# Kernel tuning notes

Measured on AMD Instinct MI355X. Metric: run time of the kernel, lower is better.

Reference implementation:

```python
import jax, jax.numpy as jnp
import numpy as np

NH = 16  # matches init kwarg nh


def setup_inputs() -> dict:
    key = jax.random.key(0)
    k1, k2 = jax.random.split(key)
    b, S, T = 4, 4096, 4096
    x = jax.random.normal(k1, (b, S, 1), dtype=jnp.float32)
    coords_rel = jax.random.normal(k2, (2, b, S, T), dtype=jnp.float32)
    return {"x": x, "coords_rel": coords_rel}


def reference(x, coords_rel):
    # coords_rel: [2, b, S, T]; x: [b, S, 1]
    d = jnp.sqrt(coords_rel[0] ** 2 + coords_rel[1] ** 2)            # [b, S, T]
    # torch.topk(d, NH, dim=1, largest=False): smallest NH along source dim, ascending
    neg_vals, idx = jax.lax.top_k(jnp.transpose(-d, (0, 2, 1)), NH)  # [b, T, NH]
    dist_abs = jnp.transpose(-neg_vals, (0, 2, 1))                   # [b, NH, T]
    indices = jnp.transpose(idx, (0, 2, 1))                          # [b, NH, T]
    b, nh, t = dist_abs.shape
    w = 1.0 / (dist_abs + 1e-15) ** 2                                # [b, nh, t]
    denom = w.sum(axis=2)                                            # [b, nh] (sum over t, as in source)
    # faithful reproduction of torch .view(t,b,nh) raw reinterpretation + broadcast divide + .view(b,t,nh)
    w = (w.reshape(t, b, nh) / denom).reshape(b, t, nh)              # [b, t, nh]
    S = x.shape[1]
    idx_btn = indices.reshape(b, t, nh)                              # raw reshape, matches torch .view
    # gather: out[i,j,k] = x[i, idx[i,j,k], 0]  (x.repeat over last dim makes all columns equal)
    xg = jnp.take_along_axis(jnp.broadcast_to(x, (b, S, nh)), idx_btn, axis=1)  # [b, t, nh]
    out = (xg * w).sum(axis=2)                                       # [b, t]
    return out[..., None]                                            # [b, t, 1]
```

## Files before the change

kernel.cpp:

```cpp
#include <hip/hip_runtime.h>

#define B_ 4
#define S_ 4096
#define T_ 4096
#define NH_ 16
#define CPB 32
#define CPW 2
#define ROWS 64
#define NTILE (S_ / ROWS)
#define LDSP 33
#define NCG (T_ / CPB)

typedef unsigned long long u64;

__device__ __forceinline__ float dpp_shr1_f(float v) {
    return __int_as_float(__builtin_amdgcn_update_dpp(
        0, __float_as_int(v), 0x111 , 0xF, 0xF, true));
}
__device__ __forceinline__ int dpp_shr1_i(int v) {
    return __builtin_amdgcn_update_dpp(0, v, 0x111, 0xF, 0xF, true);
}

__global__ __launch_bounds__(1024, 8) void topk_scan(
    const float* __restrict__ coords,
    float* __restrict__ outW,
    int*   __restrict__ outI,
    float* __restrict__ partials)
{
    __shared__ float lds[2][2][ROWS * LDSP];
    __shared__ float red[16 * NH_];

    const int bid  = blockIdx.x;
    const int b    = bid >> 7;
    const int c0   = (bid & (NCG - 1)) * CPB;
    const int tid  = threadIdx.x;
    const int w    = tid >> 6;
    const int lane = tid & 63;

    const size_t plane = (size_t)B_ * S_ * T_;
    const int stid = tid & 511;
    const int srow = stid >> 3;
    const int scol = (stid & 7) * 4;
    const int pl   = (tid >= 512) ? 1 : 0;
    const float* gp = coords + (size_t)b * S_ * T_ + (size_t)srow * T_ + (c0 + scol)
                    + (pl ? plane : (size_t)0);
    float* w0 = &lds[0][pl][srow * LDSP + scol];
    float* w1 = &lds[1][pl][srow * LDSP + scol];

    float lv[CPW]; int li[CPW]; float tau[CPW];
#pragma unroll
    for (int cc = 0; cc < CPW; ++cc) {
        lv[cc]  = __int_as_float(0x7f800000);
        li[cc]  = 0;
        tau[cc] = __int_as_float(0x7f800000);
    }

    float4 r4 = *(const float4*)gp;
    w0[0] = r4.x; w0[1] = r4.y; w0[2] = r4.z; w0[3] = r4.w;
    r4 = *(const float4*)(gp + (size_t)ROWS * T_);
    __syncthreads();

#pragma unroll 1
    for (int k = 0; k < NTILE; ++k) {
        if (k + 1 < NTILE) {
            float* wb = (k & 1) ? w0 : w1;
            wb[0] = r4.x; wb[1] = r4.y; wb[2] = r4.z; wb[3] = r4.w;
        }
        if (k + 2 < NTILE)
            r4 = *(const float4*)(gp + (size_t)(k + 2) * ROWS * T_);

        const float* rb0 = lds[k & 1][0];
        const float* rb1 = lds[k & 1][1];
#pragma unroll
        for (int cc = 0; cc < CPW; ++cc) {
            const int col = w * CPW + cc;
            const float dx = rb0[lane * LDSP + col];
            const float dy = rb1[lane * LDSP + col];
            const float d2 = __fadd_rn(__fmul_rn(dx, dx), __fmul_rn(dy, dy));
            u64 m = __ballot(d2 < tau[cc]);
            while (m) {
                const int src = __ffsll(m) - 1;
                m &= m - 1;
                const float cd = __shfl(d2, src);
                const int   ci = k * ROWS + src;
                const unsigned pm = (unsigned)__ballot(lv[cc] <= cd) & 0xFFFFu;
                const int p = __popc(pm);
                const float uv = dpp_shr1_f(lv[cc]);
                const int   ui = dpp_shr1_i(li[cc]);
                const bool here  = (lane == p);
                const bool shift = (lane > p) && (lane < NH_);
                lv[cc] = here ? cd : (shift ? uv : lv[cc]);
                li[cc] = here ? ci : (shift ? ui : li[cc]);
                tau[cc] = __builtin_amdgcn_readlane(__float_as_int(lv[cc]), NH_ - 1)
                              == 0 ? 0.0f : __int_as_float(
                          __builtin_amdgcn_readlane(__float_as_int(lv[cc]), NH_ - 1));
                m &= __ballot(d2 < tau[cc]);
            }
        }
        __syncthreads();
    }

    float dsum = 0.f;
#pragma unroll
    for (int cc = 0; cc < CPW; ++cc) {
        const int t = c0 + w * CPW + cc;
        if (lane < NH_) {
            const float d = sqrtf(lv[cc]) + 1e-15f;
            const float wv = 1.0f / (d * d);
            outW[((size_t)b * T_ + t) * NH_ + lane] = wv;
            outI[((size_t)b * T_ + t) * NH_ + lane] = li[cc];
            dsum += wv;
        }
    }
    if (lane < NH_) red[w * NH_ + lane] = dsum;
    __syncthreads();
    if (tid < NH_) {
        float s = 0.f;
#pragma unroll
        for (int q = 0; q < 16; ++q) s += red[q * NH_ + tid];
        partials[(size_t)bid * NH_ + tid] = s;
    }
}

__global__ __launch_bounds__(128) void denom_reduce(
    const float* __restrict__ partials, float* __restrict__ denom)
{
    const int q = blockIdx.x;
    const int b = q >> 4, j = q & 15;
    const int g = threadIdx.x;
    __shared__ float sm[128];
    sm[g] = partials[(size_t)(b * NCG + g) * NH_ + j];
    __syncthreads();
    for (int s = 64; s > 0; s >>= 1) {
        if (g < s) sm[g] += sm[g + s];
        __syncthreads();
    }
    if (g == 0) denom[q] = sm[0];
}

__global__ __launch_bounds__(256) void out_kernel(
    const float* __restrict__ x,
    const float* __restrict__ outW,
    const int*   __restrict__ outI,
    const float* __restrict__ denom,
    float* __restrict__ out)
{
    const int gid = blockIdx.x * 256 + threadIdx.x;
    const int i = gid >> 12;
    const int j = gid & 4095;
    const int ih = j >> 8;
    const size_t base = ((size_t)i * T_ + (size_t)(j & 255) * NH_) * NH_ + ih;
    const int dq = (j & 3) * NH_;
    float acc = 0.f;
#pragma unroll
    for (int k = 0; k < NH_; ++k) {
        float w  = outW[base + (size_t)k * NH_];
        int   id = outI[base + (size_t)k * NH_];
        acc += x[i * S_ + id] * w / denom[dq + k];
    }
    out[gid] = acc;
}

extern "C" void kernel_launch(void* const* d_in, const int* in_sizes, int n_in,
                              void* d_out, int out_size, void* d_ws, size_t ws_size,
                              hipStream_t stream) {
    const float* x      = (const float*)d_in[0];
    const float* coords = (const float*)d_in[1];
    float* out = (float*)d_out;

    float* outW     = (float*)d_ws;
    int*   outI     = (int*)(outW + (size_t)B_ * T_ * NH_);
    float* partials = (float*)(outI + (size_t)B_ * T_ * NH_);
    float* denom    = partials + (size_t)(B_ * NCG) * NH_;

    topk_scan   <<<B_ * NCG,      1024, 0, stream>>>(coords, outW, outI, partials);
    denom_reduce<<<64,            128,  0, stream>>>(partials, denom);
    out_kernel  <<<B_ * T_ / 256, 256,  0, stream>>>(x, outW, outI, denom, out);
}
```

Baseline: 144.8 us.

## Compute squared distances at staging time and parallelize output reduction across lanes

The staging threads (now only the first 512) load both coordinate planes, compute dx*dx+dy*dy and write a single distance tile to LDS. This halves the LDS footprint and the per-wave LDS reads in the scan. The candidate broadcast now uses readlane instead of shfl, and the redundant tau zero check is removed. The output kernel uses 16 threads per output with a shuffle reduction, replacing the serial 16-element loop, which launches more threads but exposes more memory parallelism for the gathers.

```diff
diff --git a/kernel.cpp b/kernel.cpp
--- a/kernel.cpp
+++ b/kernel.cpp
@@ -27,7 +27,7 @@
     int*   __restrict__ outI,
     float* __restrict__ partials)
 {
-    __shared__ float lds[2][2][ROWS * LDSP];
+    __shared__ float lds[2][ROWS * LDSP];
     __shared__ float red[16 * NH_];
 
     const int bid  = blockIdx.x;
@@ -38,14 +38,13 @@
     const int lane = tid & 63;
 
     const size_t plane = (size_t)B_ * S_ * T_;
-    const int stid = tid & 511;
-    const int srow = stid >> 3;
-    const int scol = (stid & 7) * 4;
-    const int pl   = (tid >= 512) ? 1 : 0;
-    const float* gp = coords + (size_t)b * S_ * T_ + (size_t)srow * T_ + (c0 + scol)
-                    + (pl ? plane : (size_t)0);
-    float* w0 = &lds[0][pl][srow * LDSP + scol];
-    float* w1 = &lds[1][pl][srow * LDSP + scol];
+    const bool stager = (tid < 512);
+    const int  srow = tid >> 3;
+    const int  scol = (tid & 7) * 4;
+    const float* g0 = coords + (size_t)b * S_ * T_ + (size_t)srow * T_ + (c0 + scol);
+    const float* g1 = g0 + plane;
+    float* wb0 = &lds[0][srow * LDSP + scol];
+    float* wb1 = &lds[1][srow * LDSP + scol];
 
     float lv[CPW]; int li[CPW]; float tau[CPW];
 #pragma unroll
@@ -55,33 +54,45 @@
         tau[cc] = __int_as_float(0x7f800000);
     }
 
-    float4 r4 = *(const float4*)gp;
-    w0[0] = r4.x; w0[1] = r4.y; w0[2] = r4.z; w0[3] = r4.w;
-    r4 = *(const float4*)(gp + (size_t)ROWS * T_);
+    float4 ax, ay;
+    if (stager) {
+        ax = *(const float4*)g0;  ay = *(const float4*)g1;
+        wb0[0] = __fadd_rn(__fmul_rn(ax.x, ax.x), __fmul_rn(ay.x, ay.x));
+        wb0[1] = __fadd_rn(__fmul_rn(ax.y, ax.y), __fmul_rn(ay.y, ay.y));
+        wb0[2] = __fadd_rn(__fmul_rn(ax.z, ax.z), __fmul_rn(ay.z, ay.z));
+        wb0[3] = __fadd_rn(__fmul_rn(ax.w, ax.w), __fmul_rn(ay.w, ay.w));
+        ax = *(const float4*)(g0 + (size_t)ROWS * T_);
+        ay = *(const float4*)(g1 + (size_t)ROWS * T_);
+    }
     __syncthreads();
 
 #pragma unroll 1
     for (int k = 0; k < NTILE; ++k) {
-        if (k + 1 < NTILE) {
-            float* wb = (k & 1) ? w0 : w1;
-            wb[0] = r4.x; wb[1] = r4.y; wb[2] = r4.z; wb[3] = r4.w;
+        if (stager) {
+            if (k + 1 < NTILE) {
+                float* wb = (k & 1) ? wb0 : wb1;
+                wb[0] = __fadd_rn(__fmul_rn(ax.x, ax.x), __fmul_rn(ay.x, ay.x));
+                wb[1] = __fadd_rn(__fmul_rn(ax.y, ax.y), __fmul_rn(ay.y, ay.y));
+                wb[2] = __fadd_rn(__fmul_rn(ax.z, ax.z), __fmul_rn(ay.z, ay.z));
+                wb[3] = __fadd_rn(__fmul_rn(ax.w, ax.w), __fmul_rn(ay.w, ay.w));
+            }
+            if (k + 2 < NTILE) {
+                ax = *(const float4*)(g0 + (size_t)(k + 2) * ROWS * T_);
+                ay = *(const float4*)(g1 + (size_t)(k + 2) * ROWS * T_);
+            }
         }
-        if (k + 2 < NTILE)
-            r4 = *(const float4*)(gp + (size_t)(k + 2) * ROWS * T_);
 
-        const float* rb0 = lds[k & 1][0];
-        const float* rb1 = lds[k & 1][1];
+        const float* rb = lds[k & 1];
 #pragma unroll
         for (int cc = 0; cc < CPW; ++cc) {
             const int col = w * CPW + cc;
-            const float dx = rb0[lane * LDSP + col];
-            const float dy = rb1[lane * LDSP + col];
-            const float d2 = __fadd_rn(__fmul_rn(dx, dx), __fmul_rn(dy, dy));
+            const float d2 = rb[lane * LDSP + col];
             u64 m = __ballot(d2 < tau[cc]);
             while (m) {
                 const int src = __ffsll(m) - 1;
                 m &= m - 1;
-                const float cd = __shfl(d2, src);
+                const float cd = __int_as_float(
+                    __builtin_amdgcn_readlane(__float_as_int(d2), src));
                 const int   ci = k * ROWS + src;
                 const unsigned pm = (unsigned)__ballot(lv[cc] <= cd) & 0xFFFFu;
                 const int p = __popc(pm);
@@ -91,9 +102,8 @@
                 const bool shift = (lane > p) && (lane < NH_);
                 lv[cc] = here ? cd : (shift ? uv : lv[cc]);
                 li[cc] = here ? ci : (shift ? ui : li[cc]);
-                tau[cc] = __builtin_amdgcn_readlane(__float_as_int(lv[cc]), NH_ - 1)
-                              == 0 ? 0.0f : __int_as_float(
-                          __builtin_amdgcn_readlane(__float_as_int(lv[cc]), NH_ - 1));
+                tau[cc] = __int_as_float(
+                    __builtin_amdgcn_readlane(__float_as_int(lv[cc]), NH_ - 1));
                 m &= __ballot(d2 < tau[cc]);
             }
         }
@@ -145,20 +155,21 @@
     const float* __restrict__ denom,
     float* __restrict__ out)
 {
-    const int gid = blockIdx.x * 256 + threadIdx.x;
-    const int i = gid >> 12;
-    const int j = gid & 4095;
+    const int gid16 = blockIdx.x * 256 + threadIdx.x;
+    const int oid = gid16 >> 4;
+    const int q   = gid16 & 15;
+    const int i = oid >> 12;
+    const int j = oid & 4095;
     const int ih = j >> 8;
     const size_t base = ((size_t)i * T_ + (size_t)(j & 255) * NH_) * NH_ + ih;
-    const int dq = (j & 3) * NH_;
-    float acc = 0.f;
-#pragma unroll
-    for (int k = 0; k < NH_; ++k) {
-        float w  = outW[base + (size_t)k * NH_];
-        int   id = outI[base + (size_t)k * NH_];
-        acc += x[i * S_ + id] * w / denom[dq + k];
-    }
-    out[gid] = acc;
+    const float w  = outW[base + (size_t)q * NH_];
+    const int   id = outI[base + (size_t)q * NH_];
+    float v = x[i * S_ + id] * w / denom[(j & 3) * NH_ + q];
+    v += __shfl_xor(v, 1);
+    v += __shfl_xor(v, 2);
+    v += __shfl_xor(v, 4);
+    v += __shfl_xor(v, 8);
+    if (q == 0) out[oid] = v;
 }
 
 extern "C" void kernel_launch(void* const* d_in, const int* in_sizes, int n_in,
@@ -173,7 +184,7 @@
     float* partials = (float*)(outI + (size_t)B_ * T_ * NH_);
     float* denom    = partials + (size_t)(B_ * NCG) * NH_;
 
-    topk_scan   <<<B_ * NCG,      1024, 0, stream>>>(coords, outW, outI, partials);
-    denom_reduce<<<64,            128,  0, stream>>>(partials, denom);
-    out_kernel  <<<B_ * T_ / 256, 256,  0, stream>>>(x, outW, outI, denom, out);
+    topk_scan   <<<B_ * NCG,           1024, 0, stream>>>(coords, outW, outI, partials);
+    denom_reduce<<<64,                 128,  0, stream>>>(partials, denom);
+    out_kernel  <<<B_ * T_ * 16 / 256, 256,  0, stream>>>(x, outW, outI, denom, out);
 }
```

After: 131.2 us. 9.4% less time.
